# Optimization experiments

Hardware: AMD Instinct MI355X
Metric: run time of the kernel (lower is better)

The kernel has to match this reference:

```python
import jax, jax.numpy as jnp
import numpy as np

B, T, C, H, E, K = 4, 1024, 1024, 16, 8, 2
HID = 4 * C

def _ln(x, g, b, eps=1e-5):
    m = jnp.mean(x, -1, keepdims=True)
    v = jnp.mean((x - m) ** 2, -1, keepdims=True)
    return (x - m) * jax.lax.rsqrt(v + eps) * g + b

def setup_inputs() -> dict:
    key = jax.random.key(0)
    ks = jax.random.split(key, 8)
    s = 0.02
    return {
        "x": jax.random.normal(ks[0], (B, T, C), jnp.float32),
        "attention_mask": jnp.ones((B, T), jnp.int32),
        "Wq": jax.random.normal(ks[1], (C, C), jnp.float32) * s,
        "bq": jnp.zeros((C,), jnp.float32),
        "Wk": jax.random.normal(ks[2], (C, C), jnp.float32) * s,
        "bk": jnp.zeros((C,), jnp.float32),
        "Wv": jax.random.normal(ks[3], (C, C), jnp.float32) * s,
        "bv": jnp.zeros((C,), jnp.float32),
        "Wo": jax.random.normal(ks[4], (C, C), jnp.float32) * s,
        "bo": jnp.zeros((C,), jnp.float32),
        "ln1_g": jnp.ones((C,), jnp.float32),
        "ln1_b": jnp.zeros((C,), jnp.float32),
        "ln2_g": jnp.ones((C,), jnp.float32),
        "ln2_b": jnp.zeros((C,), jnp.float32),
        "Wr": jax.random.normal(ks[5], (C, E), jnp.float32) * s,
        "br": jnp.zeros((E,), jnp.float32),
        "W1": jax.random.normal(ks[6], (E, C, HID), jnp.float32) * s,
        "b1": jnp.zeros((E, HID), jnp.float32),
        "W2": jax.random.normal(ks[7], (E, HID, C), jnp.float32) * s,
        "b2": jnp.zeros((E, C), jnp.float32),
    }

def reference(x, attention_mask, Wq, bq, Wk, bk, Wv, bv, Wo, bo,
              ln1_g, ln1_b, ln2_g, ln2_b, Wr, br, W1, b1, W2, b2):
    b, t, c = x.shape
    d = c // H
    # --- multi-head self-attention with causal + padding mask ---
    q = (x @ Wq + bq).reshape(b, t, H, d).transpose(0, 2, 1, 3)  # bhtd
    k = (x @ Wk + bk).reshape(b, t, H, d).transpose(0, 2, 1, 3)
    v = (x @ Wv + bv).reshape(b, t, H, d).transpose(0, 2, 1, 3)
    scores = jnp.einsum('bhqd,bhkd->bhqk', q, k) * (1.0 / jnp.sqrt(jnp.float32(d)))
    causal = jnp.tril(jnp.ones((t, t), bool))[None, None]            # [1,1,T,T]
    mask = causal & (attention_mask[:, None, None, :] > 0)          # [B,1,T,T]
    scores = jnp.where(mask, scores, jnp.float32(-1e9))
    attn = jax.nn.softmax(scores, axis=-1)
    o = jnp.einsum('bhqk,bhkd->bhqd', attn, v).transpose(0, 2, 1, 3).reshape(b, t, c)
    mha_out = o @ Wo + bo
    x1 = _ln(x + mha_out, ln1_g, ln1_b)
    # --- sparse MoE: router -> top-k gates -> expert MLPs -> combine ---
    logits = x1 @ Wr + br                               # [B,T,E]
    probs = jax.nn.softmax(logits, axis=-1)
    _, topi = jax.lax.top_k(logits, K)                  # [B,T,K]
    emask = jnp.any(topi[..., None] == jnp.arange(E), axis=-2)  # [B,T,E] bool
    gates = jax.nn.softmax(jnp.where(emask, logits, jnp.float32(-1e9)), axis=-1)
    h = jax.nn.relu(jnp.einsum('btc,ech->bteh', x1, W1) + b1)   # [B,T,E,4C]
    oe = jnp.einsum('bteh,ehc->btec', h, W2) + b2               # [B,T,E,C]
    moe_out = jnp.einsum('btec,bte->btc', oe, gates)
    # load-balancing aux loss: E * sum(mean_prob_e * frac_routed_e)
    importance = probs.mean((0, 1))
    load = emask.astype(probs.dtype).mean((0, 1))
    lb_loss = jnp.float32(E) * jnp.sum(importance * load)
    x2 = _ln(x1 + moe_out, ln2_g, ln2_b)
    return (x2, lb_loss)
```

## Files before the change

kernel.cpp:

```cpp
#include <hip/hip_runtime.h>
#include <hip/hip_bf16.h>

typedef unsigned short u16;
typedef unsigned int u32;
typedef unsigned long long u64;
typedef __attribute__((ext_vector_type(8))) _Float16 half8;
typedef __attribute__((ext_vector_type(8))) short short8;
typedef __attribute__((ext_vector_type(4))) float f32x4;
typedef __attribute__((ext_vector_type(16))) float f32x16;
typedef __attribute__((ext_vector_type(4))) int int4v;

#define DEVI __device__ __forceinline__

static constexpr int TOK = 4096;
static constexpr int CCD = 1024;
static constexpr int HIDD = 4096;
static constexpr int MAXMT = 32;

DEVI u16 f2bf(float f) {
  u32 u = __builtin_bit_cast(u32, f);
  u32 r = (u + 0x7fffu + ((u >> 16) & 1u)) >> 16;
  return (u16)r;
}
DEVI float bf2f(u16 v) { u32 u = ((u32)v) << 16; return __builtin_bit_cast(float, u); }
DEVI u32 pkh2(_Float16 a, _Float16 b) {
  u16 ua = __builtin_bit_cast(u16, a), ub = __builtin_bit_cast(u16, b);
  return (u32)ua | ((u32)ub << 16);
}
union H8U { u32 u[4]; half8 h; };
DEVI f32x16 zero16() { f32x16 z;
#pragma unroll
  for (int i = 0; i < 16; ++i) z[i] = 0.f;
  return z; }
DEVI f32x4 zero4() { f32x4 z;
#pragma unroll
  for (int i = 0; i < 4; ++i) z[i] = 0.f;
  return z; }

DEVI void gload16(const void* g, void* l) {
  __builtin_amdgcn_global_load_lds(
      (const __attribute__((address_space(1))) void*)g,
      (__attribute__((address_space(3))) void*)l, 16, 0, 0);
}

__global__ __launch_bounds__(256) void cast_split_kernel(
    const float* __restrict__ x, _Float16* __restrict__ xh, _Float16* __restrict__ xl) {
  int i = blockIdx.x * 256 + threadIdx.x;
  float4 v = ((const float4*)x)[i];
  _Float16 h0 = (_Float16)v.x, h1 = (_Float16)v.y, h2 = (_Float16)v.z, h3 = (_Float16)v.w;
  _Float16 l0 = (_Float16)(v.x - (float)h0), l1 = (_Float16)(v.y - (float)h1);
  _Float16 l2 = (_Float16)(v.z - (float)h2), l3 = (_Float16)(v.w - (float)h3);
  ((uint2*)xh)[i] = make_uint2(pkh2(h0, h1), pkh2(h2, h3));
  ((uint2*)xl)[i] = make_uint2(pkh2(l0, l1), pkh2(l2, l3));
}

__global__ __launch_bounds__(256) void trans_split_kernel(
    const float* __restrict__ in, _Float16* __restrict__ oh, _Float16* __restrict__ ol,
    int K, int N) {
  __shared__ float tile[32][33];
  int k0 = blockIdx.x * 32, n0 = blockIdx.y * 32;
  int tx = threadIdx.x & 31, ty = threadIdx.x >> 5;
#pragma unroll
  for (int i = 0; i < 4; ++i) { int r = ty + i * 8; tile[r][tx] = in[(size_t)(k0 + r) * N + n0 + tx]; }
  __syncthreads();
#pragma unroll
  for (int i = 0; i < 4; ++i) {
    int r = ty + i * 8;
    float v = tile[tx][r];
    _Float16 h = (_Float16)v;
    oh[(size_t)(n0 + r) * K + k0 + tx] = h;
    ol[(size_t)(n0 + r) * K + k0 + tx] = (_Float16)(v - (float)h);
  }
}

__global__ __launch_bounds__(256) void trans_bf16_kernel(
    const float* __restrict__ in, u16* __restrict__ ob, int K, int N) {
  __shared__ float tile[64][33];
  in += (size_t)blockIdx.z * K * N;
  ob += (size_t)blockIdx.z * K * N;
  int k0 = blockIdx.x * 64, n0 = blockIdx.y * 32;
  int tx = threadIdx.x & 31, ty = threadIdx.x >> 5;
#pragma unroll
  for (int i = 0; i < 8; ++i) {
    int k = ty + i * 8;
    tile[k][tx] = in[(size_t)(k0 + k) * N + n0 + tx];
  }
  __syncthreads();
  int n = threadIdx.x >> 3, kc = (threadIdx.x & 7) * 8;
  short8 sv;
#pragma unroll
  for (int j = 0; j < 8; ++j) sv[j] = (short)f2bf(tile[kc + j][n]);
  *(short8*)(ob + (size_t)(n0 + n) * K + k0 + kc) = sv;
}

__global__ __launch_bounds__(256) void vtrans_kernel(
    const _Float16* __restrict__ vh, const _Float16* __restrict__ vl,
    _Float16* __restrict__ vth, _Float16* __restrict__ vtl) {
  __shared__ u32 t0[64][17], t1[64][17];
  size_t base = (size_t)blockIdx.z * 65536;
  int r0 = blockIdx.x * 64;
  int c0 = blockIdx.y * 32;
  int tx = threadIdx.x & 15, ty = threadIdx.x >> 4;
#pragma unroll
  for (int i = 0; i < 4; ++i) {
    int t = ty + i * 16;
    t0[t][tx] = *(const u32*)(vh + base + (size_t)(r0 + t) * 64 + c0 + tx * 2);
    t1[t][tx] = *(const u32*)(vl + base + (size_t)(r0 + t) * 64 + c0 + tx * 2);
  }
  __syncthreads();
  int d = threadIdx.x >> 3, tc = (threadIdx.x & 7) * 8;
  short8 sa, sb;
#pragma unroll
  for (int j = 0; j < 8; ++j) {
    u32 w0 = t0[tc + j][d >> 1], w1 = t1[tc + j][d >> 1];
    sa[j] = (short)((d & 1) ? (w0 >> 16) : (w0 & 0xffffu));
    sb[j] = (short)((d & 1) ? (w1 >> 16) : (w1 & 0xffffu));
  }
  size_t dst = base + (size_t)(c0 + d) * 1024 + r0 + tc;
  *(short8*)((u16*)vth + dst) = sa;
  *(short8*)((u16*)vtl + dst) = sb;
}

template <int EPI>
__global__ __launch_bounds__(512, 4) void gemm_f16x3_kernel(
    const _Float16* __restrict__ Ah, const _Float16* __restrict__ Al,
    const _Float16* __restrict__ Bh, const _Float16* __restrict__ Bl,
    const float* __restrict__ bias0, const float* __restrict__ bias1, const float* __restrict__ bias2,
    _Float16* __restrict__ q_h, _Float16* __restrict__ q_l,
    _Float16* __restrict__ k_h, _Float16* __restrict__ k_l,
    _Float16* __restrict__ v_h, _Float16* __restrict__ v_l,
    float* __restrict__ outf, int M, int N, int K) {
  __shared__ __align__(16) _Float16 sA[2][128 * 64];
  __shared__ __align__(16) _Float16 sB[2][128 * 64];
  const int tid = threadIdx.x;
  const int mt = blockIdx.x, nt = blockIdx.y;
  const int lane = tid & 63, wv = tid >> 6;
  const int wm = wv >> 2, wn = wv & 3;
  f32x4 acc[4][2];
#pragma unroll
  for (int m = 0; m < 4; ++m)
#pragma unroll
    for (int n = 0; n < 2; ++n) acc[m][n] = zero4();

  const _Float16* aS[2]; const _Float16* bS[2];
#pragma unroll
  for (int j = 0; j < 2; ++j) {
    int flat = j * 512 + tid;
    int row = flat >> 3, sg = flat & 7, s = sg ^ (row & 7), g = s >> 1, hl = s & 1;
    aS[j] = (hl ? Al : Ah) + (size_t)(mt * 128 + row) * K + g * 8;
    bS[j] = (hl ? Bl : Bh) + (size_t)(nt * 128 + row) * K + g * 8;
  }

  const int nkt = K >> 5;
#pragma unroll
  for (int j = 0; j < 2; ++j) gload16(aS[j], (char*)sA[0] + (j * 512 + tid) * 16);
#pragma unroll
  for (int j = 0; j < 2; ++j) gload16(bS[j], (char*)sB[0] + (j * 512 + tid) * 16);

  for (int kt = 0; kt < nkt; ++kt) {
    const int cur = kt & 1;
    if (kt + 1 < nkt) {
#pragma unroll
      for (int j = 0; j < 2; ++j) gload16(aS[j] + (kt + 1) * 32, (char*)sA[cur ^ 1] + (j * 512 + tid) * 16);
#pragma unroll
      for (int j = 0; j < 2; ++j) gload16(bS[j] + (kt + 1) * 32, (char*)sB[cur ^ 1] + (j * 512 + tid) * 16);
      asm volatile("s_waitcnt vmcnt(4)" ::: "memory");
    } else {
      asm volatile("s_waitcnt vmcnt(0)" ::: "memory");
    }
    __builtin_amdgcn_s_barrier();
    const int g2 = (lane >> 4) << 1;
    half8 bhf[2], blf[2];
#pragma unroll
    for (int n = 0; n < 2; ++n) {
      int row = wn * 32 + n * 16 + (lane & 15);
      const char* base = (const char*)sB[cur] + row * 128;
      bhf[n] = *(const half8*)(base + (((g2) ^ (row & 7)) << 4));
      blf[n] = *(const half8*)(base + (((g2 + 1) ^ (row & 7)) << 4));
    }
    __builtin_amdgcn_s_setprio(1);
#pragma unroll
    for (int m = 0; m < 4; ++m) {
      int row = wm * 64 + m * 16 + (lane & 15);
      const char* base = (const char*)sA[cur] + row * 128;
      half8 af = *(const half8*)(base + (((g2) ^ (row & 7)) << 4));
      half8 alf = *(const half8*)(base + (((g2 + 1) ^ (row & 7)) << 4));
#pragma unroll
      for (int n = 0; n < 2; ++n) {
        acc[m][n] = __builtin_amdgcn_mfma_f32_16x16x32_f16(af, bhf[n], acc[m][n], 0, 0, 0);
        acc[m][n] = __builtin_amdgcn_mfma_f32_16x16x32_f16(af, blf[n], acc[m][n], 0, 0, 0);
        acc[m][n] = __builtin_amdgcn_mfma_f32_16x16x32_f16(alf, bhf[n], acc[m][n], 0, 0, 0);
      }
    }
    __builtin_amdgcn_s_setprio(0);
    __builtin_amdgcn_s_barrier();
  }
#pragma unroll
  for (int m = 0; m < 4; ++m) {
    int lrow = wm * 64 + m * 16 + ((lane >> 4) << 2);
#pragma unroll
    for (int n = 0; n < 2; ++n) {
      int gcol = nt * 128 + wn * 32 + n * 16 + (lane & 15);
      f32x4 a = acc[m][n];
#pragma unroll
      for (int j = 0; j < 4; ++j) {
        int grow = mt * 128 + lrow + j;
        float v = a[j];
        if (EPI == 0) {
          int sec = gcol >> 10, cc = gcol & 1023;
          v += (sec == 0 ? bias0[cc] : (sec == 1 ? bias1[cc] : bias2[cc]));
          int hh = cc >> 6, dd = cc & 63;
          int bb = grow >> 10, tt = grow & 1023;
          size_t dst = (((size_t)(bb * 16 + hh)) * 1024 + tt) * 64 + dd;
          _Float16 hi = (_Float16)v;
          _Float16 lo = (_Float16)(v - (float)hi);
          if (sec == 0) { q_h[dst] = hi; q_l[dst] = lo; }
          else if (sec == 1) { k_h[dst] = hi; k_l[dst] = lo; }
          else { v_h[dst] = hi; v_l[dst] = lo; }
        } else {
          v += bias0[gcol];
          outf[(size_t)grow * N + gcol] = v;
        }
      }
    }
  }
}

__global__ __launch_bounds__(256) void attn_kernel(
    const _Float16* __restrict__ qhp, const _Float16* __restrict__ qlp,
    const _Float16* __restrict__ khp, const _Float16* __restrict__ klp,
    const _Float16* __restrict__ vth, const _Float16* __restrict__ vtl,
    const int* __restrict__ amask,
    _Float16* __restrict__ ohp, _Float16* __restrict__ olp) {
  const int lane = threadIdx.x & 63;
  const int wv = threadIdx.x >> 6;
  const int bh = blockIdx.x >> 3;
  const int qblk = (blockIdx.x & 7) + wv * 8;
  const int b = bh >> 4, hh = bh & 15;
  const int q0 = qblk * 32;
  const int qln = lane & 31;
  const int qq = q0 + qln;
  const int hf = lane >> 5;
  __shared__ float lmadd[1024];
  for (int i = threadIdx.x; i < 1024; i += 256) lmadd[i] = (amask[b * 1024 + i] > 0) ? 0.f : -1e9f;
  __syncthreads();

  size_t qoff = ((size_t)bh * 1024 + qq) * 64 + hf * 8;
  half8 qfh[4], qfl[4];
#pragma unroll
  for (int d = 0; d < 4; ++d) {
    qfh[d] = *(const half8*)(qhp + qoff + d * 16);
    qfl[d] = *(const half8*)(qlp + qoff + d * 16);
  }
  f32x16 o0 = zero16(), o1 = zero16();
  float mrun = -3.0e38f, lsum = 0.f;
  const float LOG2E = 1.44269504088896f;

  for (int kb = 0; kb <= qblk; ++kb) {
    size_t koff = ((size_t)bh * 1024 + kb * 32 + qln) * 64 + hf * 8;
    f32x16 s = zero16();
#pragma unroll
    for (int d = 0; d < 4; ++d) {
      half8 kfh = *(const half8*)(khp + koff + d * 16);
      half8 kfl = *(const half8*)(klp + koff + d * 16);
      s = __builtin_amdgcn_mfma_f32_32x32x16_f16(kfh, qfh[d], s, 0, 0, 0);
      s = __builtin_amdgcn_mfma_f32_32x32x16_f16(kfh, qfl[d], s, 0, 0, 0);
      s = __builtin_amdgcn_mfma_f32_32x32x16_f16(kfl, qfh[d], s, 0, 0, 0);
    }
    float sc[16];
#pragma unroll
    for (int r = 0; r < 16; ++r) {
      int krow = (r & 3) + ((r >> 2) << 3) + (hf << 2);
      int key = kb * 32 + krow;
      sc[r] = s[r] * 0.125f + lmadd[key];
    }
    if (kb == qblk) {
#pragma unroll
      for (int r = 0; r < 16; ++r) {
        int krow = (r & 3) + ((r >> 2) << 3) + (hf << 2);
        if (kb * 32 + krow > qq) sc[r] = -1e9f;
      }
    }
    float pm = sc[0];
#pragma unroll
    for (int r = 1; r < 16; ++r) pm = fmaxf(pm, sc[r]);
    pm = fmaxf(pm, __shfl_xor(pm, 32));
    float mnew = fmaxf(mrun, pm);
    float aold = exp2f((mrun - mnew) * LOG2E);
    float p[16]; float psum = 0.f;
#pragma unroll
    for (int r = 0; r < 16; ++r) { p[r] = exp2f((sc[r] - mnew) * LOG2E); psum += p[r]; }
    lsum = lsum * aold + psum;
#pragma unroll
    for (int j = 0; j < 16; ++j) { o0[j] *= aold; o1[j] *= aold; }
    mrun = mnew;
    u32 hd[8], ld[8];
#pragma unroll
    for (int i = 0; i < 8; ++i) {
      _Float16 h0 = (_Float16)p[2 * i], h1 = (_Float16)p[2 * i + 1];
      hd[i] = pkh2(h0, h1);
      ld[i] = pkh2((_Float16)(p[2 * i] - (float)h0), (_Float16)(p[2 * i + 1] - (float)h1));
    }
    auto mkfrag = [&](u32 d0, u32 d1, u32 d2, u32 d3) -> half8 {
      u32 e0 = (u32)__shfl_xor((int)d0, 32);
      u32 e1 = (u32)__shfl_xor((int)d1, 32);
      u32 e2 = (u32)__shfl_xor((int)d2, 32);
      u32 e3 = (u32)__shfl_xor((int)d3, 32);
      H8U t;
      t.u[0] = hf ? e2 : d0;
      t.u[1] = hf ? e3 : d1;
      t.u[2] = hf ? d2 : e0;
      t.u[3] = hf ? d3 : e1;
      return t.h;
    };
    half8 pbh0 = mkfrag(hd[0], hd[1], hd[2], hd[3]);
    half8 pbl0 = mkfrag(ld[0], ld[1], ld[2], ld[3]);
    half8 pbh1 = mkfrag(hd[4], hd[5], hd[6], hd[7]);
    half8 pbl1 = mkfrag(ld[4], ld[5], ld[6], ld[7]);
    size_t vb = ((size_t)bh * 64 + qln) * 1024 + kb * 32 + hf * 8;
    half8 vh00 = *(const half8*)(vth + vb);
    half8 vh01 = *(const half8*)(vth + vb + 16);
    half8 vh10 = *(const half8*)(vth + vb + 32 * 1024);
    half8 vh11 = *(const half8*)(vth + vb + 32 * 1024 + 16);
    half8 vl00 = *(const half8*)(vtl + vb);
    half8 vl01 = *(const half8*)(vtl + vb + 16);
    half8 vl10 = *(const half8*)(vtl + vb + 32 * 1024);
    half8 vl11 = *(const half8*)(vtl + vb + 32 * 1024 + 16);
    o0 = __builtin_amdgcn_mfma_f32_32x32x16_f16(vh00, pbh0, o0, 0, 0, 0);
    o0 = __builtin_amdgcn_mfma_f32_32x32x16_f16(vh00, pbl0, o0, 0, 0, 0);
    o0 = __builtin_amdgcn_mfma_f32_32x32x16_f16(vl00, pbh0, o0, 0, 0, 0);
    o0 = __builtin_amdgcn_mfma_f32_32x32x16_f16(vh01, pbh1, o0, 0, 0, 0);
    o0 = __builtin_amdgcn_mfma_f32_32x32x16_f16(vh01, pbl1, o0, 0, 0, 0);
    o0 = __builtin_amdgcn_mfma_f32_32x32x16_f16(vl01, pbh1, o0, 0, 0, 0);
    o1 = __builtin_amdgcn_mfma_f32_32x32x16_f16(vh10, pbh0, o1, 0, 0, 0);
    o1 = __builtin_amdgcn_mfma_f32_32x32x16_f16(vh10, pbl0, o1, 0, 0, 0);
    o1 = __builtin_amdgcn_mfma_f32_32x32x16_f16(vl10, pbh0, o1, 0, 0, 0);
    o1 = __builtin_amdgcn_mfma_f32_32x32x16_f16(vh11, pbh1, o1, 0, 0, 0);
    o1 = __builtin_amdgcn_mfma_f32_32x32x16_f16(vh11, pbl1, o1, 0, 0, 0);
    o1 = __builtin_amdgcn_mfma_f32_32x32x16_f16(vl11, pbh1, o1, 0, 0, 0);
  }
  lsum += __shfl_xor(lsum, 32);
  float inv = 1.f / lsum;
  size_t obase = ((size_t)(b * 1024 + qq)) * 1024 + hh * 64;
#pragma unroll
  for (int dt = 0; dt < 2; ++dt) {
#pragma unroll
    for (int c = 0; c < 4; ++c) {
      int dloc = dt * 32 + c * 8 + hf * 4;
      float v0, v1, v2, v3;
      if (dt == 0) { v0 = o0[4 * c] * inv; v1 = o0[4 * c + 1] * inv; v2 = o0[4 * c + 2] * inv; v3 = o0[4 * c + 3] * inv; }
      else { v0 = o1[4 * c] * inv; v1 = o1[4 * c + 1] * inv; v2 = o1[4 * c + 2] * inv; v3 = o1[4 * c + 3] * inv; }
      _Float16 h0 = (_Float16)v0, h1 = (_Float16)v1, h2 = (_Float16)v2, h3 = (_Float16)v3;
      *(uint2*)(ohp + obase + dloc) = make_uint2(pkh2(h0, h1), pkh2(h2, h3));
      *(uint2*)(olp + obase + dloc) = make_uint2(
          pkh2((_Float16)(v0 - (float)h0), (_Float16)(v1 - (float)h1)),
          pkh2((_Float16)(v2 - (float)h2), (_Float16)(v3 - (float)h3)));
    }
  }
}

__global__ __launch_bounds__(256) void ln1_kernel(
    const float* __restrict__ x, const float* __restrict__ mha,
    const float* __restrict__ gam, const float* __restrict__ bet,
    float* __restrict__ x1f, u16* __restrict__ x1b) {
  int t = blockIdx.x, tid = threadIdx.x;
  const float* xr = x + (size_t)t * 1024;
  const float* mr = mha + (size_t)t * 1024;
  float v[4], s = 0.f, ss = 0.f;
#pragma unroll
  for (int i = 0; i < 4; ++i) { int c = tid + i * 256; float a = xr[c] + mr[c]; v[i] = a; s += a; ss += a * a; }
#pragma unroll
  for (int o = 32; o; o >>= 1) { s += __shfl_xor(s, o); ss += __shfl_xor(ss, o); }
  __shared__ float rs[4], rss[4];
  int wv = tid >> 6;
  if ((tid & 63) == 0) { rs[wv] = s; rss[wv] = ss; }
  __syncthreads();
  s = rs[0] + rs[1] + rs[2] + rs[3];
  ss = rss[0] + rss[1] + rss[2] + rss[3];
  float mean = s * (1.f / 1024.f);
  float var = ss * (1.f / 1024.f) - mean * mean;
  float rstd = rsqrtf(var + 1e-5f);
#pragma unroll
  for (int i = 0; i < 4; ++i) {
    int c = tid + i * 256;
    float y = (v[i] - mean) * rstd * gam[c] + bet[c];
    x1f[(size_t)t * 1024 + c] = y;
    x1b[(size_t)t * 1024 + c] = f2bf(y);
  }
}

__global__ __launch_bounds__(256) void router_kernel(
    const float* __restrict__ x1f, const float* __restrict__ Wr, const float* __restrict__ br,
    int* __restrict__ eids, float* __restrict__ gatesv, float* __restrict__ probbuf) {
  int wv = threadIdx.x >> 6, lane = threadIdx.x & 63;
  int t = blockIdx.x * 4 + wv;
  const float* xr = x1f + (size_t)t * 1024;
  float acc[8];
#pragma unroll
  for (int e = 0; e < 8; ++e) acc[e] = 0.f;
  for (int c = lane; c < 1024; c += 64) {
    float xv = xr[c];
    const float* wr = Wr + c * 8;
#pragma unroll
    for (int e = 0; e < 8; ++e) acc[e] += xv * wr[e];
  }
#pragma unroll
  for (int e = 0; e < 8; ++e) {
#pragma unroll
    for (int o = 32; o; o >>= 1) acc[e] += __shfl_xor(acc[e], o);
    acc[e] += br[e];
  }
  if (lane == 0) {
    float mx = acc[0];
#pragma unroll
    for (int e = 1; e < 8; ++e) mx = fmaxf(mx, acc[e]);
    float pe[8], se = 0.f;
#pragma unroll
    for (int e = 0; e < 8; ++e) { pe[e] = expf(acc[e] - mx); se += pe[e]; }
    float inv = 1.f / se;
#pragma unroll
    for (int e = 0; e < 8; ++e) probbuf[(size_t)t * 8 + e] = pe[e] * inv;
    int i0 = 0;
#pragma unroll
    for (int e = 1; e < 8; ++e) if (acc[e] > acc[i0]) i0 = e;
    int i1 = -1;
#pragma unroll
    for (int e = 0; e < 8; ++e) if (e != i0 && (i1 < 0 || acc[e] > acc[i1])) i1 = e;
    float m2 = fmaxf(acc[i0], acc[i1]);
    float g0 = expf(acc[i0] - m2), g1 = expf(acc[i1] - m2);
    float gs = 1.f / (g0 + g1);
    eids[t * 2] = i0; eids[t * 2 + 1] = i1;
    gatesv[t * 2] = g0 * gs; gatesv[t * 2 + 1] = g1 * gs;
  }
}

__global__ __launch_bounds__(256) void count_offs_kernel(
    const int* __restrict__ eids, int* __restrict__ counts, int* __restrict__ offs) {
  __shared__ int lc[8];
  if (threadIdx.x < 8) lc[threadIdx.x] = 0;
  __syncthreads();
  for (int i = threadIdx.x; i < TOK * 2; i += 256) atomicAdd(&lc[eids[i]], 1);
  __syncthreads();
  if (threadIdx.x == 0) {
    int s = 0;
#pragma unroll
    for (int e = 0; e < 8; ++e) { counts[e] = lc[e]; offs[e] = s; s += lc[e]; }
    offs[8] = s;
  }
}

__global__ __launch_bounds__(256) void scatter_kernel(
    const int* __restrict__ eids, const int* __restrict__ offs, int* __restrict__ cursor,
    int* __restrict__ tlist, int* __restrict__ invx) {
  int t = blockIdx.x * 256 + threadIdx.x;
  int lane = threadIdx.x & 63;
#pragma unroll
  for (int s = 0; s < 2; ++s) {
    int e = eids[t * 2 + s];
#pragma unroll
    for (int ex = 0; ex < 8; ++ex) {
      u64 m = __ballot(e == ex);
      if (e == ex) {
        int leader = __ffsll((long long)m) - 1;
        int rank = __popcll(m & ((1ull << lane) - 1ull));
        int base = 0;
        if (lane == leader) base = atomicAdd(&cursor[ex], __popcll(m));
        base = __shfl(base, leader);
        int idx = offs[ex] + base + rank;
        tlist[idx] = t;
        invx[t * 2 + s] = idx;
      }
    }
  }
}

template <int EPI>
__global__ __launch_bounds__(512, 4) void gemm_bf16_kernel(
    const u16* __restrict__ Abase, const u16* __restrict__ Bbase, const float* __restrict__ bias,
    u16* __restrict__ outb, float* __restrict__ outf,
    const int* __restrict__ tlist, const int* __restrict__ offs,
    int K, int ldA, int N, int NTILES) {
  int bid = blockIdx.x;
  int e = bid / (MAXMT * NTILES);
  int rem = bid % (MAXMT * NTILES);
  int mt = rem / NTILES, nt = rem % NTILES;
  int mstart = offs[e], mend = offs[e + 1];
  int ne = mend - mstart;
  if (mt * 128 >= ne) return;
  const int half = blockIdx.y;
  const int kOff = half * K;
  const u16* Bt = Bbase + (size_t)e * N * ldA;
  const float* bvec = bias + (size_t)e * N;
  __shared__ __align__(16) u16 sA[3][128 * 32];
  __shared__ __align__(16) u16 sB[3][128 * 32];
  const int tid = threadIdx.x;
  const int lane = tid & 63, wv = tid >> 6;
  const int wm = wv >> 2, wn = wv & 3;
  f32x4 acc[4][2];
#pragma unroll
  for (int m = 0; m < 4; ++m)
#pragma unroll
    for (int n = 0; n < 2; ++n) acc[m][n] = zero4();

  const int row = tid >> 2, sg = tid & 3, g = sg ^ (row & 3);
  int rl = mt * 128 + row;
  if (rl >= ne) rl = ne - 1;
  size_t arow = (EPI == 2) ? (size_t)tlist[mstart + rl] : (size_t)(mstart + rl);
  const u16* aS = Abase + arow * ldA + kOff + g * 8;
  const u16* bS = Bt + (size_t)(nt * 128 + row) * ldA + kOff + g * 8;

  const int nkt = K >> 5;
  gload16(aS, (char*)sA[0] + tid * 16);
  gload16(bS, (char*)sB[0] + tid * 16);
  gload16(aS + 32, (char*)sA[1] + tid * 16);
  gload16(bS + 32, (char*)sB[1] + tid * 16);

  int slot = 0;
  for (int kt = 0; kt < nkt; ++kt) {
    if (kt + 2 < nkt) {
      int ps = slot + 2; if (ps >= 3) ps -= 3;
      gload16(aS + (kt + 2) * 32, (char*)sA[ps] + tid * 16);
      gload16(bS + (kt + 2) * 32, (char*)sB[ps] + tid * 16);
    }
    int remt = nkt - 1 - kt;
    if (remt >= 2) asm volatile("s_waitcnt vmcnt(4)" ::: "memory");
    else if (remt == 1) asm volatile("s_waitcnt vmcnt(2)" ::: "memory");
    else asm volatile("s_waitcnt vmcnt(0)" ::: "memory");
    __builtin_amdgcn_s_barrier();
    const int gg = lane >> 4;
    short8 bfr[2];
#pragma unroll
    for (int n = 0; n < 2; ++n) {
      int r2 = wn * 32 + n * 16 + (lane & 15);
      bfr[n] = *(const short8*)((const char*)sB[slot] + r2 * 64 + ((gg ^ (r2 & 3)) << 4));
    }
    __builtin_amdgcn_s_setprio(1);
#pragma unroll
    for (int m = 0; m < 4; ++m) {
      int ra = wm * 64 + m * 16 + (lane & 15);
      short8 afr = *(const short8*)((const char*)sA[slot] + ra * 64 + ((gg ^ (ra & 3)) << 4));
#pragma unroll
      for (int n = 0; n < 2; ++n)
        acc[m][n] = __builtin_amdgcn_mfma_f32_16x16x32_bf16(afr, bfr[n], acc[m][n], 0, 0, 0);
    }
    __builtin_amdgcn_s_setprio(0);
    __builtin_amdgcn_s_barrier();
    ++slot; if (slot == 3) slot = 0;
  }
#pragma unroll
  for (int m = 0; m < 4; ++m) {
    int lrow = wm * 64 + m * 16 + ((lane >> 4) << 2);
#pragma unroll
    for (int n = 0; n < 2; ++n) {
      int col = nt * 128 + wn * 32 + n * 16 + (lane & 15);
      f32x4 a = acc[m][n];
#pragma unroll
      for (int j = 0; j < 4; ++j) {
        int rl2 = mt * 128 + lrow + j;
        if (rl2 < ne) {
          size_t pair = (size_t)(mstart + rl2);
          float v = a[j] + ((EPI == 2 || half == 0) ? bvec[col] : 0.f);
          if (EPI == 2) { v = fmaxf(v, 0.f); outb[pair * N + col] = f2bf(v); }
          else outb[((size_t)half * 8192 + pair) * N + col] = f2bf(v);
        }
      }
    }
  }
}

__global__ __launch_bounds__(256) void ln2_kernel(
    const float* __restrict__ x1f, const u16* __restrict__ oe,
    const int* __restrict__ invx, const float* __restrict__ gatesv,
    const float* __restrict__ gam, const float* __restrict__ bet, float* __restrict__ out) {
  int t = blockIdx.x, tid = threadIdx.x;
  int i0 = invx[t * 2], i1 = invx[t * 2 + 1];
  float g0 = gatesv[t * 2], g1 = gatesv[t * 2 + 1];
  const u16* r0a = oe + (size_t)i0 * 1024;
  const u16* r0b = oe + (size_t)(8192 + i0) * 1024;
  const u16* r1a = oe + (size_t)i1 * 1024;
  const u16* r1b = oe + (size_t)(8192 + i1) * 1024;
  const float* xr = x1f + (size_t)t * 1024;
  float v[4], s = 0.f, ss = 0.f;
#pragma unroll
  for (int i = 0; i < 4; ++i) {
    int c = tid + i * 256;
    float a = xr[c] + g0 * (bf2f(r0a[c]) + bf2f(r0b[c])) + g1 * (bf2f(r1a[c]) + bf2f(r1b[c]));
    v[i] = a; s += a; ss += a * a;
  }
#pragma unroll
  for (int o = 32; o; o >>= 1) { s += __shfl_xor(s, o); ss += __shfl_xor(ss, o); }
  __shared__ float rs[4], rss[4];
  int wv = tid >> 6;
  if ((tid & 63) == 0) { rs[wv] = s; rss[wv] = ss; }
  __syncthreads();
  s = rs[0] + rs[1] + rs[2] + rs[3];
  ss = rss[0] + rss[1] + rss[2] + rss[3];
  float mean = s * (1.f / 1024.f);
  float var = ss * (1.f / 1024.f) - mean * mean;
  float rstd = rsqrtf(var + 1e-5f);
#pragma unroll
  for (int i = 0; i < 4; ++i) {
    int c = tid + i * 256;
    out[(size_t)t * 1024 + c] = (v[i] - mean) * rstd * gam[c] + bet[c];
  }
}

__global__ __launch_bounds__(256) void loss_kernel(
    const float* __restrict__ probbuf, const int* __restrict__ counts,
    float* __restrict__ out) {
  __shared__ float ps[256][8];
  float a[8];
#pragma unroll
  for (int e = 0; e < 8; ++e) a[e] = 0.f;
  for (int r = threadIdx.x; r < TOK; r += 256) {
#pragma unroll
    for (int e = 0; e < 8; ++e) a[e] += probbuf[(size_t)r * 8 + e];
  }
#pragma unroll
  for (int e = 0; e < 8; ++e) ps[threadIdx.x][e] = a[e];
  __syncthreads();
  if (threadIdx.x == 0) {
    float s = 0.f;
#pragma unroll
    for (int e = 0; e < 8; ++e) {
      float imp = 0.f;
      for (int i = 0; i < 256; ++i) imp += ps[i][e];
      s += (imp * (1.f / 4096.f)) * ((float)counts[e] * (1.f / 4096.f));
    }
    out[0] = 8.f * s;
  }
}

extern "C" void kernel_launch(void* const* d_in, const int* in_sizes, int n_in,
                              void* d_out, int out_size, void* d_ws, size_t ws_size,
                              hipStream_t stream) {
  const float* x = (const float*)d_in[0];
  const int* amask = (const int*)d_in[1];
  const float* Wq = (const float*)d_in[2]; const float* bq = (const float*)d_in[3];
  const float* Wk = (const float*)d_in[4]; const float* bk = (const float*)d_in[5];
  const float* Wv = (const float*)d_in[6]; const float* bv = (const float*)d_in[7];
  const float* Wo = (const float*)d_in[8]; const float* bo = (const float*)d_in[9];
  const float* g1 = (const float*)d_in[10]; const float* be1 = (const float*)d_in[11];
  const float* g2 = (const float*)d_in[12]; const float* be2 = (const float*)d_in[13];
  const float* Wr = (const float*)d_in[14]; const float* br = (const float*)d_in[15];
  const float* W1 = (const float*)d_in[16]; const float* b1 = (const float*)d_in[17];
  const float* W2 = (const float*)d_in[18]; const float* b2 = (const float*)d_in[19];
  float* out = (float*)d_out;

  char* w = (char*)d_ws;
  auto alloc = [&](size_t bytes) -> char* {
    char* p = w; w += (bytes + 255) & ~(size_t)255; return p;
  };
  _Float16* xsh = (_Float16*)alloc((size_t)TOK * CCD * 2);
  _Float16* xsl = (_Float16*)alloc((size_t)TOK * CCD * 2);
  _Float16* wqh = (_Float16*)alloc((size_t)3072 * 1024 * 2);
  _Float16* wql = (_Float16*)alloc((size_t)3072 * 1024 * 2);
  _Float16* woh = (_Float16*)alloc((size_t)1024 * 1024 * 2);
  _Float16* wol = (_Float16*)alloc((size_t)1024 * 1024 * 2);
  _Float16* qhi = (_Float16*)alloc((size_t)TOK * CCD * 2);
  _Float16* qlo = (_Float16*)alloc((size_t)TOK * CCD * 2);
  _Float16* khi = (_Float16*)alloc((size_t)TOK * CCD * 2);
  _Float16* klo = (_Float16*)alloc((size_t)TOK * CCD * 2);
  _Float16* vhi = (_Float16*)alloc((size_t)TOK * CCD * 2);
  _Float16* vlo = (_Float16*)alloc((size_t)TOK * CCD * 2);
  _Float16* vthi = (_Float16*)alloc((size_t)TOK * CCD * 2);
  _Float16* vtlo = (_Float16*)alloc((size_t)TOK * CCD * 2);
  _Float16* ohi = (_Float16*)alloc((size_t)TOK * CCD * 2);
  _Float16* olo = (_Float16*)alloc((size_t)TOK * CCD * 2);
  float* mha = (float*)alloc((size_t)TOK * CCD * 4);
  float* x1f = (float*)alloc((size_t)TOK * CCD * 4);
  u16* x1b = (u16*)alloc((size_t)TOK * CCD * 2);
  u16* w1t = (u16*)alloc((size_t)8 * HIDD * CCD * 2);
  u16* w2t = (u16*)alloc((size_t)8 * CCD * HIDD * 2);
  u16* hbuf = (u16*)alloc((size_t)8192 * HIDD * 2);
  float* probbuf = (float*)alloc((size_t)TOK * 8 * 4);
  int* eids = (int*)alloc(TOK * 2 * 4);
  float* gatesv = (float*)alloc(TOK * 2 * 4);
  int* invx = (int*)alloc(TOK * 2 * 4);
  int* tlist = (int*)alloc(8192 * 4);
  char* ctrl = alloc(4096);
  int* counts = (int*)ctrl;
  int* cursor = counts + 8;
  int* offs = counts + 16;
  u16* oe = (u16*)qhi;

  hipMemsetAsync(ctrl, 0, 256, stream);

  cast_split_kernel<<<4096, 256, 0, stream>>>(x, xsh, xsl);
  trans_split_kernel<<<dim3(32, 32), 256, 0, stream>>>(Wq, wqh, wql, 1024, 1024);
  trans_split_kernel<<<dim3(32, 32), 256, 0, stream>>>(Wk, wqh + (size_t)1024 * 1024, wql + (size_t)1024 * 1024, 1024, 1024);
  trans_split_kernel<<<dim3(32, 32), 256, 0, stream>>>(Wv, wqh + (size_t)2048 * 1024, wql + (size_t)2048 * 1024, 1024, 1024);
  trans_split_kernel<<<dim3(32, 32), 256, 0, stream>>>(Wo, woh, wol, 1024, 1024);
  trans_bf16_kernel<<<dim3(16, 128, 8), 256, 0, stream>>>(W1, w1t, 1024, 4096);
  trans_bf16_kernel<<<dim3(64, 32, 8), 256, 0, stream>>>(W2, w2t, 4096, 1024);

  gemm_f16x3_kernel<0><<<dim3(32, 24), 512, 0, stream>>>(
      xsh, xsl, wqh, wql, bq, bk, bv,
      qhi, qlo, khi, klo, vhi, vlo, nullptr, 4096, 3072, 1024);
  vtrans_kernel<<<dim3(16, 2, 64), 256, 0, stream>>>(vhi, vlo, vthi, vtlo);
  attn_kernel<<<512, 256, 0, stream>>>(qhi, qlo, khi, klo, vthi, vtlo, amask, ohi, olo);
  gemm_f16x3_kernel<1><<<dim3(32, 8), 512, 0, stream>>>(
      ohi, olo, woh, wol, bo, nullptr, nullptr,
      nullptr, nullptr, nullptr, nullptr, nullptr, nullptr, mha, 4096, 1024, 1024);
  ln1_kernel<<<4096, 256, 0, stream>>>(x, mha, g1, be1, x1f, x1b);
  router_kernel<<<1024, 256, 0, stream>>>(x1f, Wr, br, eids, gatesv, probbuf);
  count_offs_kernel<<<1, 256, 0, stream>>>(eids, counts, offs);
  scatter_kernel<<<16, 256, 0, stream>>>(eids, offs, cursor, tlist, invx);
  gemm_bf16_kernel<2><<<dim3(8 * MAXMT * 32, 1), 512, 0, stream>>>(
      x1b, w1t, b1, hbuf, nullptr, tlist, offs, 1024, 1024, 4096, 32);
  gemm_bf16_kernel<3><<<dim3(8 * MAXMT * 8, 2), 512, 0, stream>>>(
      hbuf, w2t, b2, oe, nullptr, nullptr, offs, 2048, 4096, 1024, 8);
  ln2_kernel<<<4096, 256, 0, stream>>>(x1f, oe, invx, gatesv, g2, be2, out);
  loss_kernel<<<1, 256, 0, stream>>>(probbuf, counts, out + (size_t)TOK * CCD);
}
```

Baseline: 683.0 us.

## Enlarge MoE expert GEMM tiles to 256x256 with double-buffered combined LDS

The grouped expert GEMMs move from 128x128 tiles with a triple-buffered split A/B shared-memory pipeline to 256x256 tiles. Each warp now holds 8x4 MFMA accumulators, and A and B share one double-buffered swizzled LDS buffer. The goal is higher arithmetic intensity and fewer redundant global loads per FLOP. The cost is lower occupancy (launch bounds 2), a shallower prefetch depth, more padding waste on partially filled expert tiles, and a larger register footprint.

New measurement: 762.4 us. +11.6%, slower.

```diff
diff --git a/kernel.cpp b/kernel.cpp
--- a/kernel.cpp
+++ b/kernel.cpp
@@ -15,7 +15,6 @@
 static constexpr int TOK = 4096;
 static constexpr int CCD = 1024;
 static constexpr int HIDD = 4096;
-static constexpr int MAXMT = 32;
 
 DEVI u16 f2bf(float f) {
   u32 u = __builtin_bit_cast(u32, f);
@@ -475,90 +474,92 @@
 }
 
 template <int EPI>
-__global__ __launch_bounds__(512, 4) void gemm_bf16_kernel(
+__global__ __launch_bounds__(512, 2) void gemm_bf16_kernel(
     const u16* __restrict__ Abase, const u16* __restrict__ Bbase, const float* __restrict__ bias,
-    u16* __restrict__ outb, float* __restrict__ outf,
-    const int* __restrict__ tlist, const int* __restrict__ offs,
-    int K, int ldA, int N, int NTILES) {
+    u16* __restrict__ outb, const int* __restrict__ tlist, const int* __restrict__ offs,
+    int K, int ldA, int N, int MT, int NTILES) {
   int bid = blockIdx.x;
-  int e = bid / (MAXMT * NTILES);
-  int rem = bid % (MAXMT * NTILES);
+  int e = bid / (MT * NTILES);
+  int rem = bid % (MT * NTILES);
   int mt = rem / NTILES, nt = rem % NTILES;
   int mstart = offs[e], mend = offs[e + 1];
   int ne = mend - mstart;
-  if (mt * 128 >= ne) return;
+  if (mt * 256 >= ne) return;
   const int half = blockIdx.y;
   const int kOff = half * K;
   const u16* Bt = Bbase + (size_t)e * N * ldA;
   const float* bvec = bias + (size_t)e * N;
-  __shared__ __align__(16) u16 sA[3][128 * 32];
-  __shared__ __align__(16) u16 sB[3][128 * 32];
+  __shared__ __align__(16) u16 sAB[2][256 * 64];
   const int tid = threadIdx.x;
   const int lane = tid & 63, wv = tid >> 6;
-  const int wm = wv >> 2, wn = wv & 3;
-  f32x4 acc[4][2];
-#pragma unroll
-  for (int m = 0; m < 4; ++m)
-#pragma unroll
-    for (int n = 0; n < 2; ++n) acc[m][n] = zero4();
-
-  const int row = tid >> 2, sg = tid & 3, g = sg ^ (row & 3);
-  int rl = mt * 128 + row;
-  if (rl >= ne) rl = ne - 1;
-  size_t arow = (EPI == 2) ? (size_t)tlist[mstart + rl] : (size_t)(mstart + rl);
-  const u16* aS = Abase + arow * ldA + kOff + g * 8;
-  const u16* bS = Bt + (size_t)(nt * 128 + row) * ldA + kOff + g * 8;
+  const int wr = wv >> 2, wc = wv & 3;
+  f32x4 acc[8][4];
+#pragma unroll
+  for (int m = 0; m < 8; ++m)
+#pragma unroll
+    for (int n = 0; n < 4; ++n) acc[m][n] = zero4();
+
+  const u16* src[4];
+#pragma unroll
+  for (int j = 0; j < 4; ++j) {
+    int flat = j * 512 + tid;
+    int r = flat >> 3, sg = flat & 7, v = sg ^ (r & 7);
+    int mat = v >> 2, ch = v & 3;
+    if (mat == 0) {
+      int rl = mt * 256 + r;
+      if (rl >= ne) rl = ne - 1;
+      size_t arow = (EPI == 2) ? (size_t)tlist[mstart + rl] : (size_t)(mstart + rl);
+      src[j] = Abase + arow * ldA + kOff + ch * 8;
+    } else {
+      src[j] = Bt + (size_t)(nt * 256 + r) * ldA + kOff + ch * 8;
+    }
+  }
 
   const int nkt = K >> 5;
-  gload16(aS, (char*)sA[0] + tid * 16);
-  gload16(bS, (char*)sB[0] + tid * 16);
-  gload16(aS + 32, (char*)sA[1] + tid * 16);
-  gload16(bS + 32, (char*)sB[1] + tid * 16);
-
-  int slot = 0;
+#pragma unroll
+  for (int j = 0; j < 4; ++j) gload16(src[j], (char*)sAB[0] + (j * 512 + tid) * 16);
+  asm volatile("s_waitcnt vmcnt(0)" ::: "memory");
+  __builtin_amdgcn_s_barrier();
+
   for (int kt = 0; kt < nkt; ++kt) {
-    if (kt + 2 < nkt) {
-      int ps = slot + 2; if (ps >= 3) ps -= 3;
-      gload16(aS + (kt + 2) * 32, (char*)sA[ps] + tid * 16);
-      gload16(bS + (kt + 2) * 32, (char*)sB[ps] + tid * 16);
-    }
-    int remt = nkt - 1 - kt;
-    if (remt >= 2) asm volatile("s_waitcnt vmcnt(4)" ::: "memory");
-    else if (remt == 1) asm volatile("s_waitcnt vmcnt(2)" ::: "memory");
-    else asm volatile("s_waitcnt vmcnt(0)" ::: "memory");
+    const int cur = kt & 1;
+    if (kt + 1 < nkt) {
+#pragma unroll
+      for (int j = 0; j < 4; ++j) gload16(src[j] + (kt + 1) * 32, (char*)sAB[cur ^ 1] + (j * 512 + tid) * 16);
+    }
+    const int gg = lane >> 4;
+    const char* base = (const char*)sAB[cur];
+    short8 bfr[4];
+#pragma unroll
+    for (int n = 0; n < 4; ++n) {
+      int R = wc * 64 + n * 16 + (lane & 15);
+      bfr[n] = *(const short8*)(base + R * 128 + (((4 | gg) ^ (R & 7)) << 4));
+    }
+    __builtin_amdgcn_s_setprio(1);
+#pragma unroll
+    for (int m = 0; m < 8; ++m) {
+      int R = wr * 128 + m * 16 + (lane & 15);
+      short8 afr = *(const short8*)(base + R * 128 + ((gg ^ (R & 7)) << 4));
+#pragma unroll
+      for (int n = 0; n < 4; ++n)
+        acc[m][n] = __builtin_amdgcn_mfma_f32_16x16x32_bf16(afr, bfr[n], acc[m][n], 0, 0, 0);
+    }
+    __builtin_amdgcn_s_setprio(0);
+    asm volatile("s_waitcnt vmcnt(0)" ::: "memory");
     __builtin_amdgcn_s_barrier();
-    const int gg = lane >> 4;
-    short8 bfr[2];
-#pragma unroll
-    for (int n = 0; n < 2; ++n) {
-      int r2 = wn * 32 + n * 16 + (lane & 15);
-      bfr[n] = *(const short8*)((const char*)sB[slot] + r2 * 64 + ((gg ^ (r2 & 3)) << 4));
-    }
-    __builtin_amdgcn_s_setprio(1);
-#pragma unroll
-    for (int m = 0; m < 4; ++m) {
-      int ra = wm * 64 + m * 16 + (lane & 15);
-      short8 afr = *(const short8*)((const char*)sA[slot] + ra * 64 + ((gg ^ (ra & 3)) << 4));
-#pragma unroll
-      for (int n = 0; n < 2; ++n)
-        acc[m][n] = __builtin_amdgcn_mfma_f32_16x16x32_bf16(afr, bfr[n], acc[m][n], 0, 0, 0);
-    }
-    __builtin_amdgcn_s_setprio(0);
-    __builtin_amdgcn_s_barrier();
-    ++slot; if (slot == 3) slot = 0;
-  }
-#pragma unroll
-  for (int m = 0; m < 4; ++m) {
-    int lrow = wm * 64 + m * 16 + ((lane >> 4) << 2);
-#pragma unroll
-    for (int n = 0; n < 2; ++n) {
-      int col = nt * 128 + wn * 32 + n * 16 + (lane & 15);
+  }
+#pragma unroll
+  for (int m = 0; m < 8; ++m) {
+    int lrow = wr * 128 + m * 16 + ((lane >> 4) << 2);
+#pragma unroll
+    for (int n = 0; n < 4; ++n) {
+      int col = nt * 256 + wc * 64 + n * 16 + (lane & 15);
       f32x4 a = acc[m][n];
 #pragma unroll
       for (int j = 0; j < 4; ++j) {
-        int rl2 = mt * 128 + lrow + j;
-        if (rl2 < ne) {
-          size_t pair = (size_t)(mstart + rl2);
+        int rl = mt * 256 + lrow + j;
+        if (rl < ne) {
+          size_t pair = (size_t)(mstart + rl);
           float v = a[j] + ((EPI == 2 || half == 0) ? bvec[col] : 0.f);
           if (EPI == 2) { v = fmaxf(v, 0.f); outb[pair * N + col] = f2bf(v); }
           else outb[((size_t)half * 8192 + pair) * N + col] = f2bf(v);
@@ -706,10 +707,10 @@
   router_kernel<<<1024, 256, 0, stream>>>(x1f, Wr, br, eids, gatesv, probbuf);
   count_offs_kernel<<<1, 256, 0, stream>>>(eids, counts, offs);
   scatter_kernel<<<16, 256, 0, stream>>>(eids, offs, cursor, tlist, invx);
-  gemm_bf16_kernel<2><<<dim3(8 * MAXMT * 32, 1), 512, 0, stream>>>(
-      x1b, w1t, b1, hbuf, nullptr, tlist, offs, 1024, 1024, 4096, 32);
-  gemm_bf16_kernel<3><<<dim3(8 * MAXMT * 8, 2), 512, 0, stream>>>(
-      hbuf, w2t, b2, oe, nullptr, nullptr, offs, 2048, 4096, 1024, 8);
+  gemm_bf16_kernel<2><<<dim3(8 * 16 * 16, 1), 512, 0, stream>>>(
+      x1b, w1t, b1, hbuf, tlist, offs, 1024, 1024, 4096, 16, 16);
+  gemm_bf16_kernel<3><<<dim3(8 * 16 * 4, 2), 512, 0, stream>>>(
+      hbuf, w2t, b2, oe, nullptr, offs, 2048, 4096, 1024, 16, 4);
   ln2_kernel<<<4096, 256, 0, stream>>>(x1f, oe, invx, gatesv, g2, be2, out);
   loss_kernel<<<1, 256, 0, stream>>>(probbuf, counts, out + (size_t)TOK * CCD);
 }
```
